# Kernel optimization log

Measured on AMD Instinct MI355X. Metric: run time of the kernel, lower is better.

## Reference

```python
import jax, jax.numpy as jnp
import numpy as np

SCALER = 8.0  # math.sqrt(feature_size=64), fixed at __init__


def setup_inputs() -> dict:
    key = jax.random.key(0)
    kq, kk, kv = jax.random.split(key, 3)
    B, H, S, D = 2, 16, 2048, 64
    q = jax.random.normal(kq, (B, H, S, D), dtype=jnp.float32)
    k = jax.random.normal(kk, (B, H, S, D), dtype=jnp.float32)
    v = jax.random.normal(kv, (B, H, S, D), dtype=jnp.float32)
    return {"q": q, "k": k, "v": v, "feature_size": 64}


def reference(q, k, v, feature_size):
    # scores: [B, H, Sq, Sk]
    scores = jnp.einsum("bhqd,bhkd->bhqk", q, k) / SCALER
    # nn.Softmax2d softmaxes over the CHANNEL dim (axis=1, the head dim)
    # at each (q, k) spatial location -- faithful to the original module.
    attn = jax.nn.softmax(scores, axis=1)
    # dropout p=0.0 -> identity
    out = jnp.einsum("bhqk,bhkd->bhqd", attn, v)
    return (out, attn)
```

## Files before the change

kernel.cpp:

```cpp
#include <hip/hip_runtime.h>
#include <stdint.h>

#define Bn 2
#define Hn 16
#define Sn 2048
#define Dn 64
#define TQ 16
#define KSPLIT 8
#define KRANGE (Sn / KSPLIT)
#define KITER 32
#define NITER (KRANGE / KITER)

typedef __attribute__((ext_vector_type(8))) short short8;
typedef __attribute__((ext_vector_type(4))) short short4v;
typedef __attribute__((ext_vector_type(4))) float float4v;

__device__ __forceinline__ short f2bf(float f) {
    uint32_t u = __builtin_bit_cast(uint32_t, f);
    u += 0x7fffu + ((u >> 16) & 1u);
    return (short)(u >> 16);
}
__device__ __forceinline__ float bf2f(short s) {
    uint32_t u = ((uint32_t)(uint16_t)s) << 16;
    return __builtin_bit_cast(float, u);
}
__device__ __forceinline__ short8 load_bf8(const float* p) {
    float4v a = *(const float4v*)p;
    float4v b = *(const float4v*)(p + 4);
    short8 r;
    r[0] = f2bf(a[0]); r[1] = f2bf(a[1]); r[2] = f2bf(a[2]); r[3] = f2bf(a[3]);
    r[4] = f2bf(b[0]); r[5] = f2bf(b[1]); r[6] = f2bf(b[2]); r[7] = f2bf(b[3]);
    return r;
}

#define MFMA(a, b, c) __builtin_amdgcn_mfma_f32_16x16x32_bf16((a), (b), (c), 0, 0, 0)

__global__ __launch_bounds__(512, 4) void attn_fused(
    const float* __restrict__ Q, const float* __restrict__ K,
    const float* __restrict__ V, float* __restrict__ Out,
    float* __restrict__ Attn)
{
    __shared__ short part[8][KITER][20];
    __shared__ float den[KITER][20];
    __shared__ short pbuf[8][TQ][40];

    const int bid0 = blockIdx.x;
    const int bid  = (bid0 & 7) * 256 + (bid0 >> 3);

    const int qb = bid & 127;
    const int t2 = bid >> 7;
    const int ks = t2 & 7;
    const int b  = t2 >> 3;

    const int tid  = threadIdx.x;
    const int wave = tid >> 6;
    const int lane = tid & 63;
    const int quad = lane >> 4;
    const int l16  = lane & 15;

    const int h0 = wave * 2;
    const int q0 = qb * TQ;
    const int k0 = ks * KRANGE;

    short8 aq[2][2];
#pragma unroll
    for (int hi = 0; hi < 2; ++hi) {
        const float* qp = Q + ((size_t)(b * Hn + h0 + hi) * Sn + (size_t)(q0 + l16)) * Dn
                            + quad * 8;
        aq[hi][0] = load_bf8(qp);
        aq[hi][1] = load_bf8(qp + 32);
    }

    float4v acc[2][4];
#pragma unroll
    for (int hi = 0; hi < 2; ++hi)
#pragma unroll
        for (int dc = 0; dc < 4; ++dc)
            acc[hi][dc] = (float4v){0.f, 0.f, 0.f, 0.f};

    for (int it = 0; it < NITER; ++it) {
        const int kb = k0 + it * KITER;

        float4v e[2][2];
#pragma unroll
        for (int kk = 0; kk < 2; ++kk) {
            const size_t krow = (size_t)(kb + kk * 16 + l16);
            const float* kp0 = K + ((size_t)(b * Hn + h0)     * Sn + krow) * Dn + quad * 8;
            const float* kp1 = K + ((size_t)(b * Hn + h0 + 1) * Sn + krow) * Dn + quad * 8;
            short8 b00 = load_bf8(kp0);
            short8 b01 = load_bf8(kp0 + 32);
            short8 b10 = load_bf8(kp1);
            short8 b11 = load_bf8(kp1 + 32);
            float4v c0 = (float4v){0.f, 0.f, 0.f, 0.f};
            float4v c1 = (float4v){0.f, 0.f, 0.f, 0.f};
            c0 = MFMA(aq[0][0], b00, c0); c0 = MFMA(aq[0][1], b01, c0);
            c1 = MFMA(aq[1][0], b10, c1); c1 = MFMA(aq[1][1], b11, c1);
#pragma unroll
            for (int r = 0; r < 4; ++r) {
                e[0][kk][r] = __expf(c0[r] * 0.125f);
                e[1][kk][r] = __expf(c1[r] * 0.125f);
            }
            float4v p = e[0][kk] + e[1][kk];
            short4v pb;
#pragma unroll
            for (int r = 0; r < 4; ++r) pb[r] = f2bf(p[r]);
            *(short4v*)&part[wave][kk * 16 + l16][quad * 4] = pb;
        }
        __syncthreads();

        {
            const int kkr = tid >> 4;
            const int qq  = tid & 15;
            float s = 0.f;
#pragma unroll
            for (int w = 0; w < 8; ++w) s += bf2f(part[w][kkr][qq]);
            den[kkr][qq] = s;
        }
        __syncthreads();

        float4v r4[2];
#pragma unroll
        for (int kk = 0; kk < 2; ++kk) {
            float4v d4 = *(const float4v*)&den[kk * 16 + l16][quad * 4];
#pragma unroll
            for (int r = 0; r < 4; ++r) r4[kk][r] = __builtin_amdgcn_rcpf(d4[r]);
        }

#pragma unroll
        for (int hi = 0; hi < 2; ++hi) {
            const int h = h0 + hi;
#pragma unroll
            for (int kk = 0; kk < 2; ++kk) {
                float4v a = e[hi][kk] * r4[kk];
                size_t base = ((size_t)(b * Hn + h) * Sn + (size_t)(q0 + quad * 4)) * Sn
                              + (size_t)(kb + kk * 16 + l16);
#pragma unroll
                for (int r = 0; r < 4; ++r) {
                    __builtin_nontemporal_store(a[r], Attn + base + (size_t)r * Sn);
                    pbuf[wave][quad * 4 + r][kk * 16 + l16] = f2bf(a[r]);
                }
            }
            short8 av = *(const short8*)&pbuf[wave][l16][quad * 8];
            const float* vbase = V + ((size_t)(b * Hn + h) * Sn + (size_t)(kb + quad * 8)) * Dn;
#pragma unroll
            for (int dc = 0; dc < 4; ++dc) {
                short8 bv;
#pragma unroll
                for (int j = 0; j < 8; ++j)
                    bv[j] = f2bf(vbase[(size_t)j * Dn + dc * 16 + l16]);
                acc[hi][dc] = MFMA(av, bv, acc[hi][dc]);
            }
        }
    }

#pragma unroll
    for (int hi = 0; hi < 2; ++hi)
#pragma unroll
        for (int dc = 0; dc < 4; ++dc) {
            float* op = Out + ((size_t)(b * Hn + h0 + hi) * Sn + (size_t)(q0 + quad * 4)) * Dn
                        + dc * 16 + l16;
#pragma unroll
            for (int r = 0; r < 4; ++r)
                unsafeAtomicAdd(op + (size_t)r * Dn, acc[hi][dc][r]);
        }
}

extern "C" void kernel_launch(void* const* d_in, const int* in_sizes, int n_in,
                              void* d_out, int out_size, void* d_ws, size_t ws_size,
                              hipStream_t stream) {
    const float* q = (const float*)d_in[0];
    const float* k = (const float*)d_in[1];
    const float* v = (const float*)d_in[2];
    float* out  = (float*)d_out;
    float* attn = out + (size_t)Bn * Hn * Sn * Dn;

    hipMemsetAsync(d_out, 0, (size_t)Bn * Hn * Sn * Dn * sizeof(float), stream);

    attn_fused<<<dim3(Bn * (Sn / TQ) * KSPLIT), dim3(512), 0, stream>>>(q, k, v, out, attn);
}
```

Measured before the change: 967.1 us.

## Stage all-head exp tiles in LDS per 128-key chunk and vectorize attn stores

Each block now processes keys in 128-wide chunks. Exponentials for all 16 heads go into a shared LDS buffer, and the head-sum denominator is computed from that buffer, where before it came from per-wave bf16 partial sums over 32 keys. The attn write is reorganized so each lane stores two float4 vectors per row instead of scattered scalar stores. It also switches to exp2 with a folded scale and takes fewer barriers per key. In exchange it uses much more LDS (about 78KB), which may reduce occupancy below the launch-bounds target, and it stores bf16-rounded exponentials before normalization.

```diff
diff --git a/kernel.cpp b/kernel.cpp
--- a/kernel.cpp
+++ b/kernel.cpp
@@ -8,8 +8,10 @@
 #define TQ 16
 #define KSPLIT 8
 #define KRANGE (Sn / KSPLIT)
-#define KITER 32
-#define NITER (KRANGE / KITER)
+#define KC 128
+#define NCHUNK (KRANGE / KC)
+#define EPAD 136
+#define DPAD 132
 
 typedef __attribute__((ext_vector_type(8))) short short8;
 typedef __attribute__((ext_vector_type(4))) short short4v;
@@ -34,15 +36,15 @@
 }
 
 #define MFMA(a, b, c) __builtin_amdgcn_mfma_f32_16x16x32_bf16((a), (b), (c), 0, 0, 0)
+#define EXP2S 0.18033688011112042f
 
 __global__ __launch_bounds__(512, 4) void attn_fused(
     const float* __restrict__ Q, const float* __restrict__ K,
     const float* __restrict__ V, float* __restrict__ Out,
     float* __restrict__ Attn)
 {
-    __shared__ short part[8][KITER][20];
-    __shared__ float den[KITER][20];
-    __shared__ short pbuf[8][TQ][40];
+    __shared__ short ebuf[Hn][TQ][EPAD];
+    __shared__ float den[TQ][DPAD];
 
     const int bid0 = blockIdx.x;
     const int bid  = (bid0 & 7) * 256 + (bid0 >> 3);
@@ -78,77 +80,80 @@
         for (int dc = 0; dc < 4; ++dc)
             acc[hi][dc] = (float4v){0.f, 0.f, 0.f, 0.f};
 
-    for (int it = 0; it < NITER; ++it) {
-        const int kb = k0 + it * KITER;
+    for (int chunk = 0; chunk < NCHUNK; ++chunk) {
+        const int kb = k0 + chunk * KC;
 
-        float4v e[2][2];
 #pragma unroll
-        for (int kk = 0; kk < 2; ++kk) {
-            const size_t krow = (size_t)(kb + kk * 16 + l16);
-            const float* kp0 = K + ((size_t)(b * Hn + h0)     * Sn + krow) * Dn + quad * 8;
-            const float* kp1 = K + ((size_t)(b * Hn + h0 + 1) * Sn + krow) * Dn + quad * 8;
-            short8 b00 = load_bf8(kp0);
-            short8 b01 = load_bf8(kp0 + 32);
-            short8 b10 = load_bf8(kp1);
-            short8 b11 = load_bf8(kp1 + 32);
-            float4v c0 = (float4v){0.f, 0.f, 0.f, 0.f};
-            float4v c1 = (float4v){0.f, 0.f, 0.f, 0.f};
-            c0 = MFMA(aq[0][0], b00, c0); c0 = MFMA(aq[0][1], b01, c0);
-            c1 = MFMA(aq[1][0], b10, c1); c1 = MFMA(aq[1][1], b11, c1);
+        for (int hi = 0; hi < 2; ++hi) {
+            const int h = h0 + hi;
+            const float* kbase = K + (size_t)(b * Hn + h) * Sn * Dn;
 #pragma unroll
-            for (int r = 0; r < 4; ++r) {
-                e[0][kk][r] = __expf(c0[r] * 0.125f);
-                e[1][kk][r] = __expf(c1[r] * 0.125f);
+            for (int kt = 0; kt < KC / 16; ++kt) {
+                const float* kp = kbase + (size_t)(kb + kt * 16 + l16) * Dn + quad * 8;
+                short8 bk0 = load_bf8(kp);
+                short8 bk1 = load_bf8(kp + 32);
+                float4v c = (float4v){0.f, 0.f, 0.f, 0.f};
+                c = MFMA(aq[hi][0], bk0, c);
+                c = MFMA(aq[hi][1], bk1, c);
+#pragma unroll
+                for (int r = 0; r < 4; ++r)
+                    ebuf[h][quad * 4 + r][kt * 16 + l16] =
+                        f2bf(__builtin_amdgcn_exp2f(c[r] * EXP2S));
             }
-            float4v p = e[0][kk] + e[1][kk];
-            short4v pb;
-#pragma unroll
-            for (int r = 0; r < 4; ++r) pb[r] = f2bf(p[r]);
-            *(short4v*)&part[wave][kk * 16 + l16][quad * 4] = pb;
         }
         __syncthreads();
 
         {
-            const int kkr = tid >> 4;
-            const int qq  = tid & 15;
-            float s = 0.f;
+            const int q  = tid >> 5;
+            const int k4 = (tid & 31) * 4;
+            float4v s = (float4v){0.f, 0.f, 0.f, 0.f};
 #pragma unroll
-            for (int w = 0; w < 8; ++w) s += bf2f(part[w][kkr][qq]);
-            den[kkr][qq] = s;
+            for (int h = 0; h < Hn; ++h) {
+                short4v v4 = *(const short4v*)&ebuf[h][q][k4];
+                s[0] += bf2f(v4[0]); s[1] += bf2f(v4[1]);
+                s[2] += bf2f(v4[2]); s[3] += bf2f(v4[3]);
+            }
+            *(float4v*)&den[q][k4] = s;
         }
         __syncthreads();
 
-        float4v r4[2];
 #pragma unroll
-        for (int kk = 0; kk < 2; ++kk) {
-            float4v d4 = *(const float4v*)&den[kk * 16 + l16][quad * 4];
+        for (int c2 = 0; c2 < KC / 32; ++c2) {
+            const int kk = c2 * 32 + quad * 8;
+            float4v dA = *(const float4v*)&den[l16][kk];
+            float4v dB = *(const float4v*)&den[l16][kk + 4];
+            float rc[8];
 #pragma unroll
-            for (int r = 0; r < 4; ++r) r4[kk][r] = __builtin_amdgcn_rcpf(d4[r]);
-        }
-
+            for (int j = 0; j < 4; ++j) {
+                rc[j]     = __builtin_amdgcn_rcpf(dA[j]);
+                rc[4 + j] = __builtin_amdgcn_rcpf(dB[j]);
+            }
 #pragma unroll
-        for (int hi = 0; hi < 2; ++hi) {
-            const int h = h0 + hi;
+            for (int hi = 0; hi < 2; ++hi) {
+                const int h = h0 + hi;
+                short8 ef = *(const short8*)&ebuf[h][l16][kk];
+                float4v a0, a1;
 #pragma unroll
-            for (int kk = 0; kk < 2; ++kk) {
-                float4v a = e[hi][kk] * r4[kk];
-                size_t base = ((size_t)(b * Hn + h) * Sn + (size_t)(q0 + quad * 4)) * Sn
-                              + (size_t)(kb + kk * 16 + l16);
+                for (int j = 0; j < 4; ++j) {
+                    a0[j] = bf2f(ef[j])     * rc[j];
+                    a1[j] = bf2f(ef[4 + j]) * rc[4 + j];
+                }
+                float* ap = Attn + ((size_t)(b * Hn + h) * Sn + (size_t)(q0 + l16)) * Sn
+                            + kb + kk;
+                __builtin_nontemporal_store(a0, (float4v*)ap);
+                __builtin_nontemporal_store(a1, (float4v*)ap + 1);
+                short8 av;
 #pragma unroll
-                for (int r = 0; r < 4; ++r) {
-                    __builtin_nontemporal_store(a[r], Attn + base + (size_t)r * Sn);
-                    pbuf[wave][quad * 4 + r][kk * 16 + l16] = f2bf(a[r]);
+                for (int j = 0; j < 4; ++j) { av[j] = f2bf(a0[j]); av[4 + j] = f2bf(a1[j]); }
+                const float* vbase = V + ((size_t)(b * Hn + h) * Sn + (size_t)(kb + kk)) * Dn;
+#pragma unroll
+                for (int dc = 0; dc < 4; ++dc) {
+                    short8 bv;
+#pragma unroll
+                    for (int j = 0; j < 8; ++j)
+                        bv[j] = f2bf(vbase[(size_t)j * Dn + dc * 16 + l16]);
+                    acc[hi][dc] = MFMA(av, bv, acc[hi][dc]);
                 }
-            }
-            short8 av = *(const short8*)&pbuf[wave][l16][quad * 8];
-            const float* vbase = V + ((size_t)(b * Hn + h) * Sn + (size_t)(kb + quad * 8)) * Dn;
-#pragma unroll
-            for (int dc = 0; dc < 4; ++dc) {
-                short8 bv;
-#pragma unroll
-                for (int j = 0; j < 8; ++j)
-                    bv[j] = f2bf(vbase[(size_t)j * Dn + dc * 16 + l16]);
-                acc[hi][dc] = MFMA(av, bv, acc[hi][dc]);
             }
         }
     }
```

Result: faster. 940.6 us (-2.7%).
